# Kernel optimization log

Measured on AMD Instinct MI355X. Metric: run time of the kernel, lower is better.

## Reference

```python
import jax, jax.numpy as jnp
import numpy as np

NUM_Q_HEADS = 64
NUM_KV_HEADS = 8
HEAD_DIM = 64
HIDDEN = 2880
SLIDING_WINDOW = 128
ROPE_WAVELENGTH = 10000.0
NEG_INF = jnp.float32(-1e9)


def _rope(x, start_index=0):
    # x: (b, s, n, h). yarn with scaling_factor=1.0 == standard RoPE (split-half rotate).
    s, h = x.shape[1], x.shape[-1]
    inv_freq = 1.0 / (ROPE_WAVELENGTH ** (jnp.arange(0, h, 2, dtype=jnp.float32) / h))
    pos = jnp.arange(s, dtype=jnp.float32) + start_index
    freqs = pos[:, None] * inv_freq[None, :]  # (s, h/2)
    cos = jnp.concatenate([jnp.cos(freqs), jnp.cos(freqs)], axis=-1)[None, :, None, :]
    sin = jnp.concatenate([jnp.sin(freqs), jnp.sin(freqs)], axis=-1)[None, :, None, :]
    x1, x2 = jnp.split(x, 2, axis=-1)
    rot = jnp.concatenate([-x2, x1], axis=-1)
    return x * cos + rot * sin


def setup_inputs() -> dict:
    key = jax.random.key(0)
    ks = jax.random.split(key, 9)
    b, s = 1, 2048
    scale = 0.02
    hidden_states = jax.random.normal(ks[0], (b, s, HIDDEN), jnp.float32)
    Wq = jax.random.normal(ks[1], (HIDDEN, NUM_Q_HEADS, HEAD_DIM), jnp.float32) * scale
    Wk = jax.random.normal(ks[2], (HIDDEN, NUM_KV_HEADS, HEAD_DIM), jnp.float32) * scale
    Wv = jax.random.normal(ks[3], (HIDDEN, NUM_KV_HEADS, HEAD_DIM), jnp.float32) * scale
    Wo = jax.random.normal(ks[4], (NUM_Q_HEADS, HEAD_DIM, HIDDEN), jnp.float32) * scale
    bq = jnp.zeros((NUM_Q_HEADS, HEAD_DIM), jnp.float32)
    bk = jnp.zeros((NUM_KV_HEADS, HEAD_DIM), jnp.float32)
    bv = jnp.zeros((NUM_KV_HEADS, HEAD_DIM), jnp.float32)
    bo = jnp.zeros((HIDDEN,), jnp.float32)
    sinks = jax.random.normal(ks[5], (NUM_Q_HEADS,), jnp.float32) * 0.05
    attention_mask = jnp.tril(jnp.ones((s, s), bool))[None]  # causal, (b, q, k)
    return dict(hidden_states=hidden_states, Wq=Wq, bq=bq, Wk=Wk, bk=bk, Wv=Wv,
                bv=bv, Wo=Wo, bo=bo, sinks=sinks, attention_mask=attention_mask)


def reference(hidden_states, Wq, bq, Wk, bk, Wv, bv, Wo, bo, sinks, attention_mask):
    b, s, _ = hidden_states.shape
    inv_norm = 1.0 / np.sqrt(HEAD_DIM).astype(np.float32)
    # QKV projections (EinsumDense with bias)
    q = jnp.einsum('bqm,muh->bquh', hidden_states, Wq) + bq
    k = jnp.einsum('bkm,mvh->bkvh', hidden_states, Wk) + bk
    v = jnp.einsum('bkm,mvh->bkvh', hidden_states, Wv) + bv
    # rotary_dim == head_dim (even), so RoPE applies to the full head dim
    q = _rope(q)
    k = _rope(k)
    # GQA: repeat kv heads
    groups = NUM_Q_HEADS // NUM_KV_HEADS
    k = jnp.repeat(k, groups, axis=2)
    v = jnp.repeat(v, groups, axis=2)
    scores = jnp.einsum('bquh,bkuh->buqk', q, k) * inv_norm
    # sliding-window mask: keep kv_pos >= q_pos - window
    qpos = jnp.arange(s)
    swin = qpos[None, :] >= qpos[:, None] - SLIDING_WINDOW  # (q, k)
    scores = jnp.where(swin[None, None], scores, NEG_INF)
    scores = jnp.where(attention_mask[:, None], scores, NEG_INF)
    # sink-token logit per head appended as extra kv column
    sink = jnp.broadcast_to(sinks.reshape(1, NUM_Q_HEADS, 1, 1), (b, NUM_Q_HEADS, s, 1))
    logits = jnp.concatenate([scores, sink], axis=-1)
    m = jax.lax.stop_gradient(jnp.max(logits, axis=-1, keepdims=True))
    probs = jax.nn.softmax(logits - m, axis=-1)[..., :-1]  # drop sink column
    attn = jnp.einsum('buqk,bkuh->bquh', probs, v)
    return jnp.einsum('bquh,uhm->bqm', attn, Wo) + bo
```

## Files before the change

### kernel.cpp

```cpp
#include <hip/hip_runtime.h>
#include <cstdint>

typedef __attribute__((ext_vector_type(4))) float f32x4;
typedef __attribute__((ext_vector_type(8))) short bf16x8;

#define HIDDEN 2880
#define SEQ 2048
#define QKV_N 5120
#define WIN 128

__device__ __forceinline__ ushort f2bf(float f) {
  uint32_t u = __builtin_bit_cast(uint32_t, f);
  u += 0x7fff + ((u >> 16) & 1);
  return (ushort)(u >> 16);
}
__device__ __forceinline__ float bf2f(ushort h) {
  uint32_t u = ((uint32_t)h) << 16;
  return __builtin_bit_cast(float, u);
}

__global__ void conv_kernel(const float* __restrict__ in, ushort* __restrict__ out, int n) {
  int i = (blockIdx.x * blockDim.x + threadIdx.x) * 4;
  if (i >= n) return;
  float4 v = *(const float4*)(in + i);
  ushort4 o;
  o.x = f2bf(v.x); o.y = f2bf(v.y); o.z = f2bf(v.z); o.w = f2bf(v.w);
  *(ushort4*)(out + i) = o;
}

__global__ __launch_bounds__(256) void tconv_kernel(const float* __restrict__ in, ushort* __restrict__ out,
                                                    int R, int C, int out_ld, int out_row_off) {
  __shared__ float tile[32][33];
  int c0 = blockIdx.x * 32, r0 = blockIdx.y * 32;
  int tx = threadIdx.x & 31, ty = threadIdx.x >> 5;
#pragma unroll
  for (int i = 0; i < 32; i += 8)
    tile[ty + i][tx] = in[(size_t)(r0 + ty + i) * C + c0 + tx];
  __syncthreads();
#pragma unroll
  for (int i = 0; i < 32; i += 8)
    out[(size_t)(out_row_off + c0 + ty + i) * out_ld + r0 + tx] = f2bf(tile[tx][ty + i]);
}

__global__ void biascat_kernel(const float* __restrict__ bq, const float* __restrict__ bk,
                               const float* __restrict__ bv, float* __restrict__ out) {
  int i = blockIdx.x * blockDim.x + threadIdx.x;
  if (i >= QKV_N) return;
  float v = (i < 4096) ? bq[i] : (i < 4608) ? bk[i - 4096] : bv[i - 4608];
  out[i] = v;
}

__global__ void ropetab_kernel(float2* __restrict__ tab) {
  int i = blockIdx.x * blockDim.x + threadIdx.x;
  int s = i >> 5, d = i & 31;
  float inv = powf(10000.0f, -(float)d / 32.0f);
  float f = (float)s * inv;
  tab[i] = make_float2(cosf(f), sinf(f));
}

__global__ void rope_kernel(ushort* __restrict__ buf, const float2* __restrict__ tab, int width, int total) {
  int idx = blockIdx.x * blockDim.x + threadIdx.x;
  if (idx >= total) return;
  int s = idx / width;
  int rr = idx - s * width;
  int d = rr & 63;
  ushort* p = buf + (size_t)s * QKV_N + rr;
  float x = bf2f(*p);
  float partner = __shfl_xor(x, 32, 64);
  float2 cs = tab[(s << 5) + (d & 31)];
  float o = x * cs.x + ((d < 32) ? -partner : partner) * cs.y;
  *p = f2bf(o);
}

__global__ __launch_bounds__(256) void vt_kernel(const ushort* __restrict__ qkv, ushort* __restrict__ vt) {
  __shared__ ushort tile[64][80];
  int kv0 = blockIdx.x * 64, d0 = blockIdx.y * 64;
  int t = threadIdx.x;
#pragma unroll
  for (int p = 0; p < 2; ++p) {
    int lr = p * 32 + (t >> 3);
    *(bf16x8*)&tile[lr][(t & 7) * 8] =
        *(const bf16x8*)&qkv[(size_t)(kv0 + lr) * QKV_N + 4608 + d0 + (t & 7) * 8];
  }
  __syncthreads();
#pragma unroll
  for (int p = 0; p < 2; ++p) {
    int dl = p * 32 + (t >> 3);
    bf16x8 o;
#pragma unroll
    for (int jj = 0; jj < 8; ++jj) o[jj] = (short)tile[(t & 7) * 8 + jj][dl];
    *(bf16x8*)&vt[(size_t)(d0 + dl) * 2048 + kv0 + (t & 7) * 8] = o;
  }
}

template <int BN, bool OUT_BF16, int MINW>
__global__ __launch_bounds__(512, MINW) void gemm8_kernel(
    const ushort* __restrict__ A, const ushort* __restrict__ Bt,
    const float* __restrict__ bias, void* __restrict__ Cv,
    int K, int lda, int ldb, int ldc) {
  constexpr int NFRAG = BN / 64;
  constexpr int BHALF = BN * 64;
  constexpr int BCHUNKS = BHALF / 1024;
  constexpr int BUFBYTES = 16384 + 2 * BHALF;
  __shared__ __align__(16) char ldsbuf[2 * BUFBYTES];

  const int cpx = gridDim.x >> 3;
  const int wg = ((int)blockIdx.x & 7) * cpx + ((int)blockIdx.x >> 3);
  const int mtile = wg & 15, ntile = wg >> 4;
  const int m0 = mtile * 128, n0 = ntile * BN;

  const int tid = threadIdx.x, wv = tid >> 6, l = tid & 63;
  const int wm = wv >> 2, wn = wv & 3;
  const int r = l & 15, g = l >> 4;

  const int c = l ^ ((l >> 3) & 3);
  const ushort* gA0 = A + (size_t)(m0 + wv * 16 + (c >> 2)) * lda + (c & 3) * 8;
  const ushort* gB0 = Bt + (size_t)(n0 + (c >> 2)) * ldb + (c & 3) * 8;

  const int gsw = (g * 16) ^ (((r >> 1) & 3) << 4);
  const int aOff = (wm * 64 + r) * 64 + gsw;
  const int bOff = (wn * (NFRAG * 16) + r) * 64 + gsw;

  auto sA = [&](int nb, int kg, int kh) {
    __builtin_amdgcn_global_load_lds(
        (const __attribute__((address_space(1))) void*)(const void*)(gA0 + kg),
        (__attribute__((address_space(3))) void*)&ldsbuf[nb * BUFBYTES + kh * 8192 + wv * 1024], 16, 0, 0);
  };
  auto sB = [&](int nb, int kg, int kh) {
#pragma unroll
    for (int j = 0; j < (BCHUNKS + 7) / 8; ++j) {
      int cid = j * 8 + wv;
      if (cid < BCHUNKS)
        __builtin_amdgcn_global_load_lds(
            (const __attribute__((address_space(1))) void*)(const void*)(gB0 + (size_t)cid * 16 * ldb + kg),
            (__attribute__((address_space(3))) void*)&ldsbuf[nb * BUFBYTES + 16384 + kh * BHALF + cid * 1024],
            16, 0, 0);
    }
  };

#define BAR() __builtin_amdgcn_s_barrier()
#define LGKM0()                                              \
  do {                                                       \
    asm volatile("s_waitcnt lgkmcnt(0)" ::: "memory");       \
    __builtin_amdgcn_sched_barrier(0);                       \
  } while (0)
#define WAITV0() asm volatile("s_waitcnt vmcnt(0)" ::: "memory")

  f32x4 acc[4][NFRAG] = {};
  const int nt = K >> 6;

  sA(0, 0, 0); sA(0, 32, 1); sB(0, 0, 0); sB(0, 32, 1);
  WAITV0();
  BAR();

  for (int t = 0; t < nt; ++t) {
    const int bufOff = (t & 1) * BUFBYTES;
    const int nb = (t & 1) ^ 1;
    if (t + 1 < nt) {
      const int kn = (t + 1) * 64;
      sA(nb, kn, 0); sA(nb, kn + 32, 1);
      sB(nb, kn, 0); sB(nb, kn + 32, 1);
    }
#pragma unroll
    for (int kh = 0; kh < 2; ++kh) {
      bf16x8 aq[4], bq[NFRAG];
#pragma unroll
      for (int nf = 0; nf < NFRAG; ++nf)
        bq[nf] = *(const bf16x8*)&ldsbuf[bufOff + 16384 + kh * BHALF + bOff + nf * 1024];
#pragma unroll
      for (int mi = 0; mi < 4; ++mi)
        aq[mi] = *(const bf16x8*)&ldsbuf[bufOff + kh * 8192 + aOff + mi * 1024];
      LGKM0();
      __builtin_amdgcn_s_setprio(1);
#pragma unroll
      for (int mi = 0; mi < 4; ++mi)
#pragma unroll
        for (int nf = 0; nf < NFRAG; ++nf)
          acc[mi][nf] = __builtin_amdgcn_mfma_f32_16x16x32_bf16(aq[mi], bq[nf], acc[mi][nf], 0, 0, 0);
      __builtin_amdgcn_s_setprio(0);
    }
    WAITV0();
    BAR();
  }

#pragma unroll
  for (int mf2 = 0; mf2 < 4; ++mf2) {
#pragma unroll
    for (int nf = 0; nf < NFRAG; ++nf) {
      int cc = n0 + wn * (NFRAG * 16) + nf * 16 + r;
      float b = bias[cc];
#pragma unroll
      for (int j = 0; j < 4; ++j) {
        int rrow = m0 + wm * 64 + mf2 * 16 + g * 4 + j;
        float v = acc[mf2][nf][j] + b;
        if (OUT_BF16) ((ushort*)Cv)[(size_t)rrow * ldc + cc] = f2bf(v);
        else ((float*)Cv)[(size_t)rrow * ldc + cc] = v;
      }
    }
  }
#undef BAR
#undef LGKM0
#undef WAITV0
}

__global__ __launch_bounds__(512, 4) void attn_kernel(
    const ushort* __restrict__ qkv, const ushort* __restrict__ vt,
    const float* __restrict__ sinks, ushort* __restrict__ out) {
  __shared__ __align__(16) char lds[54272];
  const int kh = blockIdx.y;
  const int q0 = blockIdx.x * 32;
  const int kvw0 = q0 - 128;
  const int tid = threadIdx.x, w = tid >> 6, l = tid & 63;
  const int r = l & 15, g = l >> 4;
  const int h = kh * 8 + w;

  if (tid < 256) ((uint32_t*)(lds + 40960))[tid] = 0;

#pragma unroll
  for (int it = 0; it < 3; ++it) {
    int c = it * 512 + tid;
    if (c < 1280) {
      {
        int row = c >> 3, ch = c & 7;
        int kv = kvw0 + row;
        bf16x8 vv = {};
        if (kv >= 0) vv = *(const bf16x8*)&qkv[(size_t)kv * QKV_N + 4096 + kh * 64 + ch * 8];
        int byte = (row * 128 + ch * 16) ^ ((row & 7) << 4);
        *(bf16x8*)(lds + byte) = vv;
      }
      {
        int row = c / 20, ch = c - (c / 20) * 20;
        int kv = kvw0 + ch * 8;
        bf16x8 vv = {};
        if (kv >= 0) vv = *(const bf16x8*)&vt[(size_t)(kh * 64 + row) * 2048 + kv];
        int byte = (row * 320 + ch * 16) ^ ((row & 7) << 4);
        *(bf16x8*)(lds + 20480 + byte) = vv;
      }
    }
  }
  __syncthreads();

  char* Pw = lds + 41984 + w * 1536;
  const float snk = sinks[h];

#pragma unroll
  for (int si = 0; si < 2; ++si) {
    const ushort* qb = &qkv[(size_t)(q0 + si * 16 + r) * QKV_N + h * 64 + g * 8];
    bf16x8 qf0 = *(const bf16x8*)qb;
    bf16x8 qf1 = *(const bf16x8*)(qb + 32);

    f32x4 S[9];
    float mx[4] = {-3e30f, -3e30f, -3e30f, -3e30f};
#pragma unroll
    for (int tt = 0; tt < 9; ++tt) {
      int kvloc = (si + tt) * 16 + r;
      int b0 = (kvloc * 128 + g * 16) ^ ((kvloc & 7) << 4);
      int b1 = (kvloc * 128 + 64 + g * 16) ^ ((kvloc & 7) << 4);
      bf16x8 kf0 = *(const bf16x8*)(lds + b0);
      bf16x8 kf1 = *(const bf16x8*)(lds + b1);
      f32x4 s = {};
      s = __builtin_amdgcn_mfma_f32_16x16x32_bf16(qf0, kf0, s, 0, 0, 0);
      s = __builtin_amdgcn_mfma_f32_16x16x32_bf16(qf1, kf1, s, 0, 0, 0);
      int kvc = kvw0 + kvloc;
#pragma unroll
      for (int j = 0; j < 4; ++j) {
        int qr = q0 + si * 16 + g * 4 + j;
        bool valid = (kvc >= 0) && (kvc <= qr) && (kvc >= qr - WIN);
        float v = valid ? s[j] * 0.125f : -1e30f;
        s[j] = v;
        mx[j] = fmaxf(mx[j], v);
      }
      S[tt] = s;
    }
#pragma unroll
    for (int off = 1; off < 16; off <<= 1)
#pragma unroll
      for (int j = 0; j < 4; ++j) mx[j] = fmaxf(mx[j], __shfl_xor(mx[j], off, 64));
    float m[4], sum[4] = {0, 0, 0, 0};
#pragma unroll
    for (int j = 0; j < 4; ++j) m[j] = fmaxf(mx[j], snk);
#pragma unroll
    for (int tt = 0; tt < 9; ++tt)
#pragma unroll
      for (int j = 0; j < 4; ++j) {
        float p = (S[tt][j] > -1e29f) ? __expf(S[tt][j] - m[j]) : 0.0f;
        S[tt][j] = p;
        sum[j] += p;
      }
#pragma unroll
    for (int off = 1; off < 16; off <<= 1)
#pragma unroll
      for (int j = 0; j < 4; ++j) sum[j] += __shfl_xor(sum[j], off, 64);
    float rinv[4];
#pragma unroll
    for (int j = 0; j < 4; ++j) rinv[j] = 1.0f / (sum[j] + __expf(snk - m[j]));

    f32x4 acc[4] = {};
#pragma unroll
    for (int ks = 0; ks < 5; ++ks) {
#pragma unroll
      for (int c2 = 0; c2 < 2; ++c2) {
        int tt = 2 * ks + c2;
#pragma unroll
        for (int j = 0; j < 4; ++j) {
          float pv = (tt <= 8) ? S[tt][j] * rinv[j] : 0.0f;
          *(ushort*)(Pw + ((g * 4 + j) * 48 + c2 * 16 + r) * 2) = f2bf(pv);
        }
      }
      bf16x8 pa = *(const bf16x8*)(Pw + (r * 48 + g * 8) * 2);
#pragma unroll
      for (int ni = 0; ni < 4; ++ni) {
        int row = ni * 16 + r;
        int byte = (row * 320 + (si * 16 + ks * 32 + g * 8) * 2) ^ ((row & 7) << 4);
        bf16x8 vb = *(const bf16x8*)(lds + 20480 + byte);
        acc[ni] = __builtin_amdgcn_mfma_f32_16x16x32_bf16(pa, vb, acc[ni], 0, 0, 0);
      }
    }
#pragma unroll
    for (int ni = 0; ni < 4; ++ni)
#pragma unroll
      for (int j = 0; j < 4; ++j)
        out[(size_t)(q0 + si * 16 + g * 4 + j) * 4096 + h * 64 + ni * 16 + r] = f2bf(acc[ni][j]);
  }
}

extern "C" void kernel_launch(void* const* d_in, const int* in_sizes, int n_in,
                              void* d_out, int out_size, void* d_ws, size_t ws_size,
                              hipStream_t stream) {
  const float* hs = (const float*)d_in[0];
  const float* Wq = (const float*)d_in[1];
  const float* bq = (const float*)d_in[2];
  const float* Wk = (const float*)d_in[3];
  const float* bk = (const float*)d_in[4];
  const float* Wv = (const float*)d_in[5];
  const float* bv = (const float*)d_in[6];
  const float* Wo = (const float*)d_in[7];
  const float* bo = (const float*)d_in[8];
  const float* sinks = (const float*)d_in[9];
  float* out = (float*)d_out;

  char* ws = (char*)d_ws;
  ushort* hs_bf   = (ushort*)(ws + 0);
  ushort* vt_g    = (ushort*)(ws + 0);
  ushort* wqkv_t  = (ushort*)(ws + 11796480);
  ushort* attn    = (ushort*)(ws + 11796480);
  ushort* wo_t    = (ushort*)(ws + 41287680);
  ushort* qkv     = (ushort*)(ws + 66453504);
  float*  bias_all= (float*)(ws + 87425024);
  float2* tab     = (float2*)(ws + 87445504);

  conv_kernel<<<5898240 / 4 / 256, 256, 0, stream>>>(hs, hs_bf, 5898240);
  tconv_kernel<<<dim3(4096 / 32, 2880 / 32), 256, 0, stream>>>(Wq, wqkv_t, 2880, 4096, 2880, 0);
  tconv_kernel<<<dim3(512 / 32, 2880 / 32), 256, 0, stream>>>(Wk, wqkv_t, 2880, 512, 2880, 4096);
  tconv_kernel<<<dim3(512 / 32, 2880 / 32), 256, 0, stream>>>(Wv, wqkv_t, 2880, 512, 2880, 4608);
  tconv_kernel<<<dim3(2880 / 32, 4096 / 32), 256, 0, stream>>>(Wo, wo_t, 4096, 2880, 4096, 0);
  biascat_kernel<<<20, 256, 0, stream>>>(bq, bk, bv, bias_all);
  ropetab_kernel<<<2048 * 32 / 256, 256, 0, stream>>>(tab);

  gemm8_kernel<320, true, 2><<<256, 512, 0, stream>>>(hs_bf, wqkv_t, bias_all, qkv,
                                                      2880, 2880, 2880, 5120);
  rope_kernel<<<8388608 / 256, 256, 0, stream>>>(qkv, tab, 4096, 8388608);
  rope_kernel<<<1048576 / 256, 256, 0, stream>>>(qkv + 4096, tab, 512, 1048576);
  vt_kernel<<<dim3(32, 8), 256, 0, stream>>>(qkv, vt_g);
  attn_kernel<<<dim3(64, 8), 512, 0, stream>>>(qkv, vt_g, sinks, attn);
  gemm8_kernel<192, false, 4><<<240, 512, 0, stream>>>(attn, wo_t, bo, out,
                                                       4096, 4096, 4096, 2880);
}
```

Baseline: 212.2 us.

## Replace 8-wave GEMM with 4-wave 128x160 tile GEMM for both projections

Replaces the templated 8-wave, 512-thread GEMM with a 4-wave, 256-thread kernel using a fixed 128x160 output tile, with each wave computing 64x80. The QKV projection now launches 512 blocks instead of 256, and the output projection launches 288 blocks with 160-wide N tiles instead of 240 blocks of 192. The A/B global-to-LDS loads are redistributed across the four waves. The aim is better occupancy and balance across CUs, at the cost of per-block reuse and a different LDS footprint per block.

```diff
diff --git a/kernel.cpp b/kernel.cpp
--- a/kernel.cpp
+++ b/kernel.cpp
@@ -93,43 +93,47 @@
   }
 }
 
-template <int BN, bool OUT_BF16, int MINW>
-__global__ __launch_bounds__(512, MINW) void gemm8_kernel(
+template <bool OUT_BF16>
+__global__ __launch_bounds__(256, 2) void gemm4w_kernel(
     const ushort* __restrict__ A, const ushort* __restrict__ Bt,
     const float* __restrict__ bias, void* __restrict__ Cv,
     int K, int lda, int ldb, int ldc) {
-  constexpr int NFRAG = BN / 64;
-  constexpr int BHALF = BN * 64;
-  constexpr int BCHUNKS = BHALF / 1024;
+  constexpr int NFRAG = 5;
+  constexpr int BHALF = 160 * 64;
+  constexpr int BCHUNKS = 10;
   constexpr int BUFBYTES = 16384 + 2 * BHALF;
   __shared__ __align__(16) char ldsbuf[2 * BUFBYTES];
 
   const int cpx = gridDim.x >> 3;
   const int wg = ((int)blockIdx.x & 7) * cpx + ((int)blockIdx.x >> 3);
   const int mtile = wg & 15, ntile = wg >> 4;
-  const int m0 = mtile * 128, n0 = ntile * BN;
+  const int m0 = mtile * 128, n0 = ntile * 160;
 
   const int tid = threadIdx.x, wv = tid >> 6, l = tid & 63;
-  const int wm = wv >> 2, wn = wv & 3;
+  const int wm = wv >> 1, wn = wv & 1;
   const int r = l & 15, g = l >> 4;
 
   const int c = l ^ ((l >> 3) & 3);
-  const ushort* gA0 = A + (size_t)(m0 + wv * 16 + (c >> 2)) * lda + (c & 3) * 8;
+  const ushort* gA0 = A + (size_t)(m0 + (c >> 2)) * lda + (c & 3) * 8;
   const ushort* gB0 = Bt + (size_t)(n0 + (c >> 2)) * ldb + (c & 3) * 8;
 
   const int gsw = (g * 16) ^ (((r >> 1) & 3) << 4);
   const int aOff = (wm * 64 + r) * 64 + gsw;
-  const int bOff = (wn * (NFRAG * 16) + r) * 64 + gsw;
+  const int bOff = (wn * 80 + r) * 64 + gsw;
 
   auto sA = [&](int nb, int kg, int kh) {
-    __builtin_amdgcn_global_load_lds(
-        (const __attribute__((address_space(1))) void*)(const void*)(gA0 + kg),
-        (__attribute__((address_space(3))) void*)&ldsbuf[nb * BUFBYTES + kh * 8192 + wv * 1024], 16, 0, 0);
+#pragma unroll
+    for (int j = 0; j < 2; ++j) {
+      int cid = j * 4 + wv;
+      __builtin_amdgcn_global_load_lds(
+          (const __attribute__((address_space(1))) void*)(const void*)(gA0 + (size_t)cid * 16 * lda + kg),
+          (__attribute__((address_space(3))) void*)&ldsbuf[nb * BUFBYTES + kh * 8192 + cid * 1024], 16, 0, 0);
+    }
   };
   auto sB = [&](int nb, int kg, int kh) {
 #pragma unroll
-    for (int j = 0; j < (BCHUNKS + 7) / 8; ++j) {
-      int cid = j * 8 + wv;
+    for (int j = 0; j < 3; ++j) {
+      int cid = j * 4 + wv;
       if (cid < BCHUNKS)
         __builtin_amdgcn_global_load_lds(
             (const __attribute__((address_space(1))) void*)(const void*)(gB0 + (size_t)cid * 16 * ldb + kg),
@@ -187,7 +191,7 @@
   for (int mf2 = 0; mf2 < 4; ++mf2) {
 #pragma unroll
     for (int nf = 0; nf < NFRAG; ++nf) {
-      int cc = n0 + wn * (NFRAG * 16) + nf * 16 + r;
+      int cc = n0 + wn * 80 + nf * 16 + r;
       float b = bias[cc];
 #pragma unroll
       for (int j = 0; j < 4; ++j) {
@@ -357,12 +361,12 @@
   biascat_kernel<<<20, 256, 0, stream>>>(bq, bk, bv, bias_all);
   ropetab_kernel<<<2048 * 32 / 256, 256, 0, stream>>>(tab);
 
-  gemm8_kernel<320, true, 2><<<256, 512, 0, stream>>>(hs_bf, wqkv_t, bias_all, qkv,
-                                                      2880, 2880, 2880, 5120);
+  gemm4w_kernel<true><<<512, 256, 0, stream>>>(hs_bf, wqkv_t, bias_all, qkv,
+                                               2880, 2880, 2880, 5120);
   rope_kernel<<<8388608 / 256, 256, 0, stream>>>(qkv, tab, 4096, 8388608);
   rope_kernel<<<1048576 / 256, 256, 0, stream>>>(qkv + 4096, tab, 512, 1048576);
   vt_kernel<<<dim3(32, 8), 256, 0, stream>>>(qkv, vt_g);
   attn_kernel<<<dim3(64, 8), 512, 0, stream>>>(qkv, vt_g, sinks, attn);
-  gemm8_kernel<192, false, 4><<<240, 512, 0, stream>>>(attn, wo_t, bo, out,
-                                                       4096, 4096, 4096, 2880);
-}
+  gemm4w_kernel<false><<<288, 256, 0, stream>>>(attn, wo_t, bo, out,
+                                                4096, 4096, 4096, 2880);
+}
```

After: 219.6 us. 3.5% more time.
